# Performance work log

Hardware: AMD Instinct MI355X
Metric: run time of the kernel (lower is better)

Reference implementation:

```python
import jax, jax.numpy as jnp
import numpy as np

D_MODEL = 2048
NUM_HEADS = 32
NUM_KV_HEADS = 8
D_K = D_MODEL // NUM_HEADS  # 64
GROUPS = NUM_HEADS // NUM_KV_HEADS  # 4
ROPE_BASE = 10000.0


def rope_cos_sin(n, dim):
    # RotaryPositionalEmbedding.forward: freqs = t outer inv_freq; emb = cat(freqs, freqs)
    inv_freq = 1.0 / (ROPE_BASE ** (jnp.arange(0, dim, 2, dtype=jnp.float32) / dim))
    t = jnp.arange(n, dtype=jnp.float32)
    freqs = jnp.einsum('i,j->ij', t, inv_freq)  # [n, dim/2]
    emb = jnp.concatenate([freqs, freqs], axis=-1)  # [n, dim]
    return jnp.cos(emb), jnp.sin(emb)


def rotate_half(x):
    x1, x2 = x[..., : x.shape[-1] // 2], x[..., x.shape[-1] // 2:]
    return jnp.concatenate([-x2, x1], axis=-1)


def setup_inputs() -> dict:
    key = jax.random.key(0)
    k0, k1, k2, k3, k4 = jax.random.split(key, 5)
    B, N = 1, 2048
    x = jax.random.normal(k0, (B, N, D_MODEL), dtype=jnp.float32)
    s = 0.02
    Wq = jax.random.normal(k1, (D_MODEL, D_MODEL), dtype=jnp.float32) * s
    Wk = jax.random.normal(k2, (D_MODEL, NUM_KV_HEADS * D_K), dtype=jnp.float32) * s
    Wv = jax.random.normal(k3, (D_MODEL, NUM_KV_HEADS * D_K), dtype=jnp.float32) * s
    Wo = jax.random.normal(k4, (D_MODEL, D_MODEL), dtype=jnp.float32) * s
    return {'x': x, 'Wq': Wq, 'Wk': Wk, 'Wv': Wv, 'Wo': Wo}


def reference(x, Wq, Wk, Wv, Wo):
    B, N, C = x.shape
    scale = D_K ** -0.5
    # projections -> [B, H, N, d_k]
    q = (x @ Wq).reshape(B, N, NUM_HEADS, D_K).transpose(0, 2, 1, 3)
    k = (x @ Wk).reshape(B, N, NUM_KV_HEADS, D_K).transpose(0, 2, 1, 3)
    v = (x @ Wv).reshape(B, N, NUM_KV_HEADS, D_K).transpose(0, 2, 1, 3)
    # GQA: repeat_interleave KV heads to match Q heads
    k = jnp.repeat(k, GROUPS, axis=1)
    v = jnp.repeat(v, GROUPS, axis=1)
    cos, sin = rope_cos_sin(N, D_K)  # [N, d_k]
    cos = cos[None, None, :, :]
    sin = sin[None, None, :, :]
    q = q * cos + rotate_half(q) * sin
    k = k * cos + rotate_half(k) * sin
    attn = jnp.einsum('bhnd,bhmd->bhnm', q, k) * scale  # [B, H, N, N]
    attn = jax.nn.softmax(attn, axis=-1)
    out = jnp.einsum('bhnm,bhmd->bhnd', attn, v)  # [B, H, N, d_k]
    out = out.transpose(0, 2, 1, 3).reshape(B, N, C)
    out = out @ Wo
    return out, attn
```

## Files before the change

### kernel.cpp

```cpp
#include <hip/hip_runtime.h>

typedef _Float16 f16x8 __attribute__((ext_vector_type(8)));
typedef _Float16 f16x4 __attribute__((ext_vector_type(4)));
typedef _Float16 f16x2 __attribute__((ext_vector_type(2)));
typedef float f32x4 __attribute__((ext_vector_type(4)));

#define NSEQ 2048
#define DMODEL 2048
#define NHEADS 32
#define NKV 8
#define DK 64
#define MFMA16(a, b, c) __builtin_amdgcn_mfma_f32_16x16x32_f16(a, b, c, 0, 0, 0)

__device__ __forceinline__ void gload16(const void* g, void* l) {
    __builtin_amdgcn_global_load_lds(
        (const __attribute__((address_space(1))) void*)g,
        (__attribute__((address_space(3))) void*)l, 16, 0, 0);
}

__global__ __launch_bounds__(256) void prep_weights(
    const float* __restrict__ x,  const float* __restrict__ Wq,
    const float* __restrict__ Wk, const float* __restrict__ Wv,
    const float* __restrict__ Wo, _Float16* __restrict__ xh,
    _Float16* __restrict__ WqkvT, _Float16* __restrict__ WoT) {
    const int z = blockIdx.z;
    const int tx = threadIdx.x, ty = threadIdx.y;
    if (z == 0) {
        int c0 = blockIdx.x * 32, r0 = blockIdx.y * 32;
#pragma unroll
        for (int i = 0; i < 4; i++) {
            int r = r0 + ty + i * 8;
            xh[(long long)r * DMODEL + c0 + tx] = (_Float16)x[(long long)r * DMODEL + c0 + tx];
        }
        return;
    }
    const float* in; _Float16* out; int C;
    if (z == 1)      { in = Wq; out = WqkvT;                        C = 2048; }
    else if (z == 2) { in = Wk; out = WqkvT + (size_t)2048 * 2048;  C = 512;  }
    else if (z == 3) { in = Wv; out = WqkvT + (size_t)2560 * 2048;  C = 512;  }
    else             { in = Wo; out = WoT;                          C = 2048; }
    int c0 = blockIdx.x * 32, r0 = blockIdx.y * 32;
    if (c0 >= C) return;
    __shared__ float tile[32][33];
#pragma unroll
    for (int i = 0; i < 4; i++) {
        int r = r0 + ty + i * 8;
        tile[ty + i * 8][tx] = in[(long long)r * C + c0 + tx];
    }
    __syncthreads();
#pragma unroll
    for (int i = 0; i < 4; i++) {
        int c = c0 + ty + i * 8;
        out[(long long)c * 2048 + r0 + tx] = (_Float16)tile[tx][ty + i * 8];
    }
}

__global__ __launch_bounds__(256) void transpose16p(const _Float16* __restrict__ in,
                                                    _Float16* __restrict__ out,
                                                    int R, int C, int pitch) {
    __shared__ _Float16 tile[32][34];
    int c0 = blockIdx.x * 32, r0 = blockIdx.y * 32;
    int tx = threadIdx.x, ty = threadIdx.y;
#pragma unroll
    for (int i = 0; i < 4; i++) {
        int r = r0 + ty + i * 8;
        tile[ty + i * 8][tx] = in[(long long)r * pitch + c0 + tx];
    }
    __syncthreads();
#pragma unroll
    for (int i = 0; i < 4; i++) {
        int c = c0 + ty + i * 8;
        out[(long long)c * R + r0 + tx] = tile[tx][ty + i * 8];
    }
}

__global__ void rope_table(float2* __restrict__ cs) {
    int idx = blockIdx.x * blockDim.x + threadIdx.x;
    int n = idx >> 5, j = idx & 31;
    float e = (2.0f * j) / 64.0f;
    float invf = 1.0f / powf(10000.0f, e);
    float ang = (float)n * invf;
    float2 v; v.x = cosf(ang); v.y = sinf(ang);
    cs[idx] = v;
}

__global__ void rope_apply16(const _Float16* __restrict__ QKV, const float2* __restrict__ cs,
                             _Float16* __restrict__ out) {
    int idx = blockIdx.x * blockDim.x + threadIdx.x;
    int n = idx >> 8, rem = idx & 255;
    int hk = rem >> 5, j = rem & 31;
    float2 c = cs[n * 32 + j];
    const _Float16* in = QKV + (long long)n * 3072 + 2048 + hk * 64;
    float x1 = (float)in[j], x2 = (float)in[j + 32];
    long long ob = (long long)n * 512 + hk * 64;
    out[ob + j]      = (_Float16)(x1 * c.x - x2 * c.y);
    out[ob + j + 32] = (_Float16)(x2 * c.x + x1 * c.y);
}

template <int BM, int BN, int MF, int NF, typename OutT>
__global__ __launch_bounds__(256) void gemm_lds2(const _Float16* __restrict__ Ap,
                                                 const _Float16* __restrict__ Bt,
                                                 OutT* __restrict__ C,
                                                 int K, int lda, int ldb, int ldc) {
    __shared__ __align__(16) _Float16 As[BM * 64];
    __shared__ __align__(16) _Float16 Bs[BN * 64];

    const int tid = threadIdx.x;
    const int lane = tid & 63, w = tid >> 6;
    constexpr int WC = BN / (NF * 16);
    const int wr = w / WC, wc = w % WC;
    const int wm = wr * MF * 16, wn = wc * NF * 16;
    const int am = lane & 15;
    const int g = lane >> 4;
    const int aswz = (am & 7) << 4;

    f32x4 acc[MF][NF] = {};

    const long long a_row0 = (long long)blockIdx.y * BM * lda;
    const long long b_row0 = (long long)blockIdx.x * BN * ldb;

    const int srow = lane >> 3;
    const int scolb = (lane & 7) * 16;

    for (int kt = 0; kt < K; kt += 64) {
#pragma unroll
        for (int q = 0; q < BM / 32; q++) {
            const int rA = w * (BM / 4) + q * 8;
            const int r = rA + srow;
            gload16(Ap + a_row0 + (long long)r * lda + kt + ((scolb ^ ((r & 7) << 4)) >> 1),
                    &As[rA * 64]);
        }
#pragma unroll
        for (int q = 0; q < BN / 32; q++) {
            const int rB = w * (BN / 4) + q * 8;
            const int r = rB + srow;
            gload16(Bt + b_row0 + (long long)r * ldb + kt + ((scolb ^ ((r & 7) << 4)) >> 1),
                    &Bs[rB * 64]);
        }
        __syncthreads();

#pragma unroll
        for (int ks = 0; ks < 2; ks++) {
            const int koff = ((ks * 64 + g * 16) ^ aswz) >> 1;
            f16x8 af[MF], bf[NF];
#pragma unroll
            for (int m = 0; m < MF; m++)
                af[m] = *(const f16x8*)&As[(wm + m * 16 + am) * 64 + koff];
#pragma unroll
            for (int n = 0; n < NF; n++)
                bf[n] = *(const f16x8*)&Bs[(wn + n * 16 + am) * 64 + koff];
#pragma unroll
            for (int m = 0; m < MF; m++)
#pragma unroll
                for (int n = 0; n < NF; n++)
                    acc[m][n] = MFMA16(af[m], bf[n], acc[m][n]);
        }
        __syncthreads();
    }

    const int rb = blockIdx.y * BM + wm + (lane >> 4) * 4;
    const int cb = blockIdx.x * BN + wn + am;
#pragma unroll
    for (int m = 0; m < MF; m++)
#pragma unroll
        for (int n = 0; n < NF; n++)
#pragma unroll
            for (int j = 0; j < 4; j++)
                C[(long long)(rb + m * 16 + j) * ldc + cb + n * 16] = (OutT)acc[m][n][j];
}

__global__ __launch_bounds__(512) void attn_sums(
    const _Float16* __restrict__ QKV,
    const float2*  __restrict__ cs,
    const _Float16* __restrict__ Kh,
    float* __restrict__ Sinv)
{
    __shared__ __align__(16) char LB[32768];

    const int h = blockIdx.y, q0 = blockIdx.x * 128;
    const int kvh = h >> 2;
    const int tid = threadIdx.x, lane = tid & 63, w = tid >> 6;
    const int g = lane >> 4, c = lane & 15;
    const int swz = (c & 7) << 4;

    const _Float16* qp = QKV + (long long)(q0 + w * 16 + c) * 3072 + h * 64;
    f16x8 q0v = *(const f16x8*)(qp + g * 8);
    f16x8 q1v = *(const f16x8*)(qp + 32 + g * 8);
    const float2* csp = cs + (q0 + w * 16 + c) * 32 + g * 8;
    f16x8 qa, qb_;
#pragma unroll
    for (int e = 0; e < 8; e++) {
        float2 cv = csp[e];
        float x1 = (float)q0v[e], x2 = (float)q1v[e];
        qa[e]  = (_Float16)(x1 * cv.x - x2 * cv.y);
        qb_[e] = (_Float16)(x2 * cv.x + x1 * cv.y);
    }

    const _Float16* Kg = Kh + kvh * 64;
    const int krl = lane >> 3, kcb = (lane & 7) * 16;

#pragma unroll
    for (int q = 0; q < 2; q++) {
        int r = w * 16 + q * 8 + krl;
        gload16(Kg + (long long)r * 512 + ((kcb ^ ((r & 7) << 4)) >> 1),
                LB + (w * 16 + q * 8) * 128);
    }
    __syncthreads();

    float l = 0.f;
    for (int i = 0; i < 16; i++) {
        const char* kbuf = LB + (i & 1) * 16384;
        char* kstage = LB + ((i & 1) ^ 1) * 16384;
        const int nkc = ((i + 1) & 15) * 128;
#pragma unroll
        for (int q = 0; q < 2; q++) {
            int r = w * 16 + q * 8 + krl;
            gload16(Kg + (long long)(nkc + r) * 512 + ((kcb ^ ((r & 7) << 4)) >> 1),
                    kstage + (w * 16 + q * 8) * 128);
        }
#pragma unroll
        for (int t = 0; t < 8; t++) {
            const char* kb = kbuf + (t * 16 + c) * 128;
            f16x8 kb0 = *(const f16x8*)(kb + ((g * 16) ^ swz));
            f16x8 kb1 = *(const f16x8*)(kb + ((64 + g * 16) ^ swz));
            f32x4 acc = {0.f, 0.f, 0.f, 0.f};
            acc = MFMA16(kb0, qa, acc);
            acc = MFMA16(kb1, qb_, acc);
            l += __expf(fminf(acc[0] * 0.125f, 11.f)) + __expf(fminf(acc[1] * 0.125f, 11.f)) +
                 __expf(fminf(acc[2] * 0.125f, 11.f)) + __expf(fminf(acc[3] * 0.125f, 11.f));
        }
        __syncthreads();
    }
    l += __shfl_xor(l, 16, 64);
    l += __shfl_xor(l, 32, 64);
    if (lane < 16)
        Sinv[(long long)h * NSEQ + q0 + w * 16 + c] = 1.0f / l;
}

__global__ __launch_bounds__(512) void fused_attn(
    const _Float16* __restrict__ QKV,
    const float2*  __restrict__ cs,
    const _Float16* __restrict__ Kh,
    const _Float16* __restrict__ Vt,
    const float* __restrict__ Sinv,
    float* __restrict__ attn,
    _Float16* __restrict__ AVh)
{
    __shared__ __align__(16) char LB[81920];

    const int h = blockIdx.y, q0 = blockIdx.x * 128;
    const int kvh = h >> 2;
    const int tid = threadIdx.x, lane = tid & 63, w = tid >> 6;
    const int g = lane >> 4, c = lane & 15;
    const int swz = (c & 7) << 4;

    const _Float16* qp = QKV + (long long)(q0 + w * 16 + c) * 3072 + h * 64;
    f16x8 q0v = *(const f16x8*)(qp + g * 8);
    f16x8 q1v = *(const f16x8*)(qp + 32 + g * 8);
    const float2* csp = cs + (q0 + w * 16 + c) * 32 + g * 8;
    f16x8 qa, qb_;
#pragma unroll
    for (int e = 0; e < 8; e++) {
        float2 cv = csp[e];
        float x1 = (float)q0v[e], x2 = (float)q1v[e];
        qa[e]  = (_Float16)(x1 * cv.x - x2 * cv.y);
        qb_[e] = (_Float16)(x2 * cv.x + x1 * cv.y);
    }

    const float inv = Sinv[(long long)h * NSEQ + q0 + w * 16 + c];

    const _Float16* Kg = Kh + kvh * 64;
    const _Float16* Vg = Vt + (long long)(kvh * 64) * NSEQ;
    char* ES = LB + 49152 + w * 4096;
    float* arow0 = attn + ((long long)h * NSEQ + q0 + w * 16) * NSEQ;

    const int krl = lane >> 3, kcb = (lane & 7) * 16;
    const int vrl = lane >> 4, vcb = (lane & 15) * 16;

#pragma unroll
    for (int q = 0; q < 2; q++) {
        int r = w * 16 + q * 8 + krl;
        gload16(Kg + (long long)r * 512 + ((kcb ^ ((r & 7) << 4)) >> 1),
                LB + (w * 16 + q * 8) * 128);
    }
#pragma unroll
    for (int q = 0; q < 2; q++) {
        int j = w + q * 8;
        int d = j * 4 + vrl;
        gload16(Vg + (long long)d * NSEQ + ((vcb ^ ((d & 7) << 4)) >> 1),
                LB + 32768 + j * 1024);
    }

    f32x4 opv[4] = {};

    for (int i = 0; i < 16; i++) {
        const int kc = i * 128;
        const char* kbuf = LB + (i & 1) * 16384;
        char* kstage = LB + ((i & 1) ^ 1) * 16384;
        const int nkc = ((i + 1) & 15) * 128;

        __syncthreads();

        if (i > 0) {
            const int pkc = kc - 128;
#pragma unroll
            for (int rr = 0; rr < 8; rr++) {
                const int r = 2 * rr + (lane >> 5);
                f16x4 ev = *(const f16x4*)(ES + r * 256 + (((lane & 31) * 8) ^ ((r & 7) << 4)));
                f32x4 o;
                o[0] = (float)ev[0]; o[1] = (float)ev[1];
                o[2] = (float)ev[2]; o[3] = (float)ev[3];
                *(f32x4*)(arow0 + (long long)r * NSEQ + pkc + (lane & 31) * 4) = o;
            }
            __asm__ volatile("s_waitcnt lgkmcnt(0)" ::: "memory");
            __builtin_amdgcn_sched_barrier(0);
        }

#pragma unroll
        for (int q = 0; q < 2; q++) {
            int r = w * 16 + q * 8 + krl;
            gload16(Kg + (long long)(nkc + r) * 512 + ((kcb ^ ((r & 7) << 4)) >> 1),
                    kstage + (w * 16 + q * 8) * 128);
        }

#pragma unroll
        for (int t = 0; t < 8; t++) {
            const char* kb = kbuf + (t * 16 + c) * 128;
            f16x8 kb0 = *(const f16x8*)(kb + ((g * 16) ^ swz));
            f16x8 kb1 = *(const f16x8*)(kb + ((64 + g * 16) ^ swz));
            f32x4 acc = {0.f, 0.f, 0.f, 0.f};
            acc = MFMA16(kb0, qa, acc);
            acc = MFMA16(kb1, qb_, acc);
            float p0 = __expf(fminf(acc[0] * 0.125f, 11.f)) * inv;
            float p1 = __expf(fminf(acc[1] * 0.125f, 11.f)) * inv;
            float p2 = __expf(fminf(acc[2] * 0.125f, 11.f)) * inv;
            float p3 = __expf(fminf(acc[3] * 0.125f, 11.f)) * inv;
            f16x2 a01; a01[0] = (_Float16)p0; a01[1] = (_Float16)p1;
            f16x2 a23; a23[0] = (_Float16)p2; a23[1] = (_Float16)p3;
            int b0 = c * 256 + ((t * 32 + g * 8) ^ swz);
            *(f16x2*)(ES + b0) = a01;
            *(f16x2*)(ES + b0 + 4) = a23;
        }
        __asm__ volatile("s_waitcnt lgkmcnt(0)" ::: "memory");
        f16x8 pa0 = *(const f16x8*)(ES + c * 256 + ((g * 16) ^ swz));
        f16x8 pa1 = *(const f16x8*)(ES + c * 256 + ((64 + g * 16) ^ swz));
        f16x8 pa2 = *(const f16x8*)(ES + c * 256 + ((128 + g * 16) ^ swz));
        f16x8 pa3 = *(const f16x8*)(ES + c * 256 + ((192 + g * 16) ^ swz));

#pragma unroll
        for (int dt = 0; dt < 4; dt++) {
            const char* vrow = LB + 32768 + (dt * 16 + c) * 256;
            f16x8 vb0 = *(const f16x8*)(vrow + ((g * 16) ^ swz));
            f16x8 vb1 = *(const f16x8*)(vrow + ((64 + g * 16) ^ swz));
            f16x8 vb2 = *(const f16x8*)(vrow + ((128 + g * 16) ^ swz));
            f16x8 vb3 = *(const f16x8*)(vrow + ((192 + g * 16) ^ swz));
            opv[dt] = MFMA16(pa0, vb0, opv[dt]);
            opv[dt] = MFMA16(pa1, vb1, opv[dt]);
            opv[dt] = MFMA16(pa2, vb2, opv[dt]);
            opv[dt] = MFMA16(pa3, vb3, opv[dt]);
        }

        __asm__ volatile("s_waitcnt lgkmcnt(0)" ::: "memory");
        __builtin_amdgcn_s_barrier();

#pragma unroll
        for (int q = 0; q < 2; q++) {
            int j = w + q * 8;
            int d = j * 4 + vrl;
            gload16(Vg + (long long)d * NSEQ + nkc + ((vcb ^ ((d & 7) << 4)) >> 1),
                    LB + 32768 + j * 1024);
        }
    }

    {
        const int pkc = 15 * 128;
#pragma unroll
        for (int rr = 0; rr < 8; rr++) {
            const int r = 2 * rr + (lane >> 5);
            f16x4 ev = *(const f16x4*)(ES + r * 256 + (((lane & 31) * 8) ^ ((r & 7) << 4)));
            f32x4 o;
            o[0] = (float)ev[0]; o[1] = (float)ev[1];
            o[2] = (float)ev[2]; o[3] = (float)ev[3];
            *(f32x4*)(arow0 + (long long)r * NSEQ + pkc + (lane & 31) * 4) = o;
        }
    }

#pragma unroll
    for (int dt = 0; dt < 4; dt++)
#pragma unroll
        for (int j = 0; j < 4; j++)
            AVh[(long long)(q0 + w * 16 + 4 * g + j) * DMODEL + h * 64 + dt * 16 + c] =
                (_Float16)opv[dt][j];
}

extern "C" void kernel_launch(void* const* d_in, const int* in_sizes, int n_in,
                              void* d_out, int out_size, void* d_ws, size_t ws_size,
                              hipStream_t stream) {
    const float* x  = (const float*)d_in[0];
    const float* Wq = (const float*)d_in[1];
    const float* Wk = (const float*)d_in[2];
    const float* Wv = (const float*)d_in[3];
    const float* Wo = (const float*)d_in[4];
    float* out = (float*)d_out;
    float* attn = out + (size_t)NSEQ * DMODEL;

    char* w = (char*)d_ws;
    auto alloc = [&](size_t bytes) { char* p = w; w += (bytes + 255) & ~(size_t)255; return p; };
    const size_t MD = (size_t)NSEQ * DMODEL;
    const size_t MKV = (size_t)NSEQ * NKV * DK;
    _Float16* xh    = (_Float16*)alloc(MD * 2);
    _Float16* WqkvT = (_Float16*)alloc((size_t)3072 * 2048 * 2);
    _Float16* WoT   = (_Float16*)alloc(MD * 2);
    float2*   cs    = (float2*)alloc((size_t)NSEQ * 32 * sizeof(float2));
    _Float16* QKV   = (_Float16*)alloc((size_t)2048 * 3072 * 2);
    _Float16* Kh    = (_Float16*)alloc(MKV * 2);
    _Float16* Vt    = (_Float16*)alloc(MKV * 2);
    float*    Sinv  = (float*)alloc((size_t)NHEADS * NSEQ * 4);
    _Float16* AVh   = xh;

    prep_weights<<<dim3(64, 64, 5), dim3(32, 8), 0, stream>>>(
        x, Wq, Wk, Wv, Wo, xh, WqkvT, WoT);
    rope_table<<<256, 256, 0, stream>>>(cs);

    gemm_lds2<128, 64, 4, 2, _Float16><<<dim3(48, 16), 256, 0, stream>>>(
        xh, WqkvT, QKV, DMODEL, DMODEL, DMODEL, 3072);

    rope_apply16<<<2048, 256, 0, stream>>>(QKV, cs, Kh);
    transpose16p<<<dim3(16, 64), dim3(32, 8), 0, stream>>>(QKV + 2560, Vt, NSEQ, 512, 3072);

    attn_sums<<<dim3(NSEQ / 128, NHEADS), 512, 0, stream>>>(QKV, cs, Kh, Sinv);

    fused_attn<<<dim3(NSEQ / 128, NHEADS), 512, 0, stream>>>(QKV, cs, Kh, Vt, Sinv, attn, AVh);

    gemm_lds2<128, 64, 4, 2, float><<<dim3(32, 16), 256, 0, stream>>>(
        AVh, WoT, out, DMODEL, DMODEL, DMODEL, DMODEL);
}
```

Measured before the change: 261.7 us.

## Double-buffer LDS tiles in projection GEMMs and remap blocks across XCDs

```diff
diff --git a/kernel.cpp b/kernel.cpp
--- a/kernel.cpp
+++ b/kernel.cpp
@@ -98,12 +98,12 @@
 }
 
 template <int BM, int BN, int MF, int NF, typename OutT>
-__global__ __launch_bounds__(256) void gemm_lds2(const _Float16* __restrict__ Ap,
+__global__ __launch_bounds__(256) void gemm_lds3(const _Float16* __restrict__ Ap,
                                                  const _Float16* __restrict__ Bt,
                                                  OutT* __restrict__ C,
                                                  int K, int lda, int ldb, int ldc) {
-    __shared__ __align__(16) _Float16 As[BM * 64];
-    __shared__ __align__(16) _Float16 Bs[BN * 64];
+    __shared__ __align__(16) _Float16 As[2][BM * 64];
+    __shared__ __align__(16) _Float16 Bs[2][BN * 64];
 
     const int tid = threadIdx.x;
     const int lane = tid & 63, w = tid >> 6;
@@ -114,30 +114,42 @@
     const int g = lane >> 4;
     const int aswz = (am & 7) << 4;
 
+    const int nwg = gridDim.x * gridDim.y;
+    int fid = blockIdx.y * gridDim.x + blockIdx.x;
+    fid = (fid & 7) * (nwg >> 3) + (fid >> 3);
+    const int bx = fid % gridDim.x, by = fid / gridDim.x;
+
     f32x4 acc[MF][NF] = {};
 
-    const long long a_row0 = (long long)blockIdx.y * BM * lda;
-    const long long b_row0 = (long long)blockIdx.x * BN * ldb;
+    const long long a_row0 = (long long)by * BM * lda;
+    const long long b_row0 = (long long)bx * BN * ldb;
 
     const int srow = lane >> 3;
     const int scolb = (lane & 7) * 16;
 
-    for (int kt = 0; kt < K; kt += 64) {
+    auto stage = [&](int kt, int buf) {
 #pragma unroll
         for (int q = 0; q < BM / 32; q++) {
             const int rA = w * (BM / 4) + q * 8;
             const int r = rA + srow;
             gload16(Ap + a_row0 + (long long)r * lda + kt + ((scolb ^ ((r & 7) << 4)) >> 1),
-                    &As[rA * 64]);
+                    &As[buf][rA * 64]);
         }
 #pragma unroll
         for (int q = 0; q < BN / 32; q++) {
             const int rB = w * (BN / 4) + q * 8;
             const int r = rB + srow;
             gload16(Bt + b_row0 + (long long)r * ldb + kt + ((scolb ^ ((r & 7) << 4)) >> 1),
-                    &Bs[rB * 64]);
-        }
+                    &Bs[buf][rB * 64]);
+        }
+    };
+
+    stage(0, 0);
+    int cur = 0;
+
+    for (int kt = 0; kt < K; kt += 64) {
         __syncthreads();
+        if (kt + 64 < K) stage(kt + 64, cur ^ 1);
 
 #pragma unroll
         for (int ks = 0; ks < 2; ks++) {
@@ -145,21 +157,21 @@
             f16x8 af[MF], bf[NF];
 #pragma unroll
             for (int m = 0; m < MF; m++)
-                af[m] = *(const f16x8*)&As[(wm + m * 16 + am) * 64 + koff];
+                af[m] = *(const f16x8*)&As[cur][(wm + m * 16 + am) * 64 + koff];
 #pragma unroll
             for (int n = 0; n < NF; n++)
-                bf[n] = *(const f16x8*)&Bs[(wn + n * 16 + am) * 64 + koff];
+                bf[n] = *(const f16x8*)&Bs[cur][(wn + n * 16 + am) * 64 + koff];
 #pragma unroll
             for (int m = 0; m < MF; m++)
 #pragma unroll
                 for (int n = 0; n < NF; n++)
                     acc[m][n] = MFMA16(af[m], bf[n], acc[m][n]);
         }
-        __syncthreads();
-    }
-
-    const int rb = blockIdx.y * BM + wm + (lane >> 4) * 4;
-    const int cb = blockIdx.x * BN + wn + am;
+        cur ^= 1;
+    }
+
+    const int rb = by * BM + wm + (lane >> 4) * 4;
+    const int cb = bx * BN + wn + am;
 #pragma unroll
     for (int m = 0; m < MF; m++)
 #pragma unroll
@@ -422,7 +434,7 @@
         x, Wq, Wk, Wv, Wo, xh, WqkvT, WoT);
     rope_table<<<256, 256, 0, stream>>>(cs);
 
-    gemm_lds2<128, 64, 4, 2, _Float16><<<dim3(48, 16), 256, 0, stream>>>(
+    gemm_lds3<128, 64, 4, 2, _Float16><<<dim3(48, 16), 256, 0, stream>>>(
         xh, WqkvT, QKV, DMODEL, DMODEL, DMODEL, 3072);
 
     rope_apply16<<<2048, 256, 0, stream>>>(QKV, cs, Kh);
@@ -432,6 +444,6 @@
 
     fused_attn<<<dim3(NSEQ / 128, NHEADS), 512, 0, stream>>>(QKV, cs, Kh, Vt, Sinv, attn, AVh);
 
-    gemm_lds2<128, 64, 4, 2, float><<<dim3(32, 16), 256, 0, stream>>>(
+    gemm_lds3<128, 64, 4, 2, float><<<dim3(32, 16), 256, 0, stream>>>(
         AVh, WoT, out, DMODEL, DMODEL, DMODEL, DMODEL);
 }
```

New measurement: 256.8 us. No clear change (-1.9%).
